# Optimization experiments

Hardware: AMD Instinct MI355X
Metric: run time of the kernel (lower is better)

Reference implementation:

```python
import jax, jax.numpy as jnp
import numpy as np
import math

B, S, E_PHI, E_F, H_F, N_HEADS = 2, 2048, 1024, 1024, 1024, 16


def setup_inputs() -> dict:
    key = jax.random.key(0)
    ks = jax.random.split(key, 7)
    return {
        "q": jax.random.normal(ks[0], (B, S, E_PHI), dtype=jnp.float32),
        "k": jax.random.normal(ks[1], (B, S, E_PHI), dtype=jnp.float32),
        "v": jax.random.normal(ks[2], (B, S, E_F), dtype=jnp.float32),
        # weights stored as [in, out]; applied as x @ W (same math as nn.Linear with W^T)
        "W_q": jax.random.normal(ks[3], (E_PHI, H_F), dtype=jnp.float32) * 0.02,
        "W_k": jax.random.normal(ks[4], (E_PHI, H_F), dtype=jnp.float32) * 0.02,
        "W_v": jax.random.normal(ks[5], (E_F, H_F), dtype=jnp.float32) * 0.02,
        "W_o": jax.random.normal(ks[6], (H_F, E_F), dtype=jnp.float32) * 0.02,
    }


def reference(q, k, v, W_q, W_k, W_v, W_o):
    Bq, Sq, _ = q.shape
    Dh = H_F // N_HEADS
    scale = 1.0 / math.sqrt(H_F)
    # projections -> [B, H, S, Dh]
    qh = (q @ W_q).reshape(Bq, Sq, N_HEADS, Dh).transpose(0, 2, 1, 3)
    kh = (k @ W_k).reshape(Bq, Sq, N_HEADS, Dh).transpose(0, 2, 1, 3)
    vh = (v @ W_v).reshape(Bq, Sq, N_HEADS, Dh).transpose(0, 2, 1, 3)
    # near-causal mask: mask out j >= i (triu incl. diagonal), EXCEPT position [0,0]
    mask = jnp.triu(jnp.ones((Sq, Sq), dtype=bool), 0).at[0, 0].set(False)
    scores = jnp.einsum('bhsd,bhtd->bhst', qh, kh) * scale  # [B,H,S,S]
    scores = jnp.where(mask, -jnp.inf, scores)
    probs = jax.nn.softmax(scores, axis=-1)  # dropout = identity (eval mode)
    out = jnp.einsum('bhst,bhtd->bhsd', probs, vh)  # [B,H,S,Dh]
    out = out.transpose(0, 2, 1, 3).reshape(Bq, Sq, H_F)
    return out @ W_o
```

## Files before the change

### kernel.cpp

```cpp
#include <hip/hip_runtime.h>
#include <type_traits>

#define S_LEN 2048
#define NHEAD 16
#define DHEAD 64
#define EMB   1024
#define NBATCH 2

typedef __bf16 bf16_t;
typedef bf16_t bf16x8 __attribute__((ext_vector_type(8)));
typedef float  f32x4  __attribute__((ext_vector_type(4)));
typedef unsigned short us_t;
typedef us_t   us8    __attribute__((ext_vector_type(8)));
typedef us_t   us4    __attribute__((ext_vector_type(4)));
typedef unsigned int u32x4 __attribute__((ext_vector_type(4)));
typedef unsigned int u32x2 __attribute__((ext_vector_type(2)));
typedef short  s16x4  __attribute__((ext_vector_type(4)));

static __device__ __forceinline__ bf16x8 ld_bf16x8(const us_t* p) {
  return __builtin_bit_cast(bf16x8, *reinterpret_cast<const us8*>(p));
}
static __device__ __forceinline__ us_t f2bf(float f) {
  bf16_t h = (bf16_t)f;
  return __builtin_bit_cast(us_t, h);
}
static __device__ __forceinline__ unsigned cvt_pk_bf16(float lo, float hi) {
  unsigned r;
  asm("v_cvt_pk_bf16_f32 %0, %1, %2" : "=v"(r) : "v"(lo), "v"(hi));
  return r;
}
#if __has_builtin(__builtin_amdgcn_exp2f)
#define EXP2(x) __builtin_amdgcn_exp2f(x)
#else
#define EXP2(x) exp2f(x)
#endif
static __device__ __forceinline__ void gload16(const void* g, void* lds) {
  __builtin_amdgcn_global_load_lds((const __attribute__((address_space(1))) void*)g,
                                   (__attribute__((address_space(3))) void*)lds,
                                   16, 0, 0);
}

__global__ __launch_bounds__(256) void prep(const float* __restrict__ W0,
                                            const float* __restrict__ W1,
                                            const float* __restrict__ W2,
                                            const float* __restrict__ W3,
                                            us_t* __restrict__ T0,
                                            us_t* __restrict__ T1,
                                            us_t* __restrict__ T2,
                                            us_t* __restrict__ T3) {
  __shared__ float tile[32][33];
  const int z = blockIdx.z;
  const float* W = (z == 0) ? W0 : (z == 1) ? W1 : (z == 2) ? W2 : W3;
  us_t* WT = (z == 0) ? T0 : (z == 1) ? T1 : (z == 2) ? T2 : T3;
  const int n0 = blockIdx.x * 32, k0 = blockIdx.y * 32;
  const int tx = threadIdx.x & 31, ty = threadIdx.x >> 5;
#pragma unroll
  for (int i = 0; i < 32; i += 8)
    tile[ty + i][tx] = W[(size_t)(k0 + ty + i) * EMB + n0 + tx];
  __syncthreads();
#pragma unroll
  for (int i = 0; i < 32; i += 8)
    WT[(size_t)(n0 + ty + i) * EMB + k0 + tx] = f2bf(tile[tx][ty + i]);
}

template<int MODE, bool AF32>
static __device__ __forceinline__ void gemm_core(const void* __restrict__ Ap,
                                                 const us_t* __restrict__ BT,
                                                 void* __restrict__ O,
                                                 int mt, int nt,
                                                 char (*As)[8192], char (*Bs)[8192]) {
  const int lane = threadIdx.x & 63;
  const int wave = threadIdx.x >> 6;
  const int wm = (wave >> 1) * 64;
  const int wn = (wave & 1) * 64;
  const int lr = lane & 15;
  const int lg = lane >> 4;

  f32x4 acc[4][4] = {};
  f32x4 ar[2][2];

  auto a_load = [&](int k0) {
#pragma unroll
    for (int i = 0; i < 2; ++i) {
      const int seg = wave * 2 + i;
      const int r = seg * 16 + (lane >> 2);
      const float* ap = (const float*)Ap + (size_t)(mt * 128 + r) * EMB + k0 + (lane & 3) * 8;
      ar[i][0] = *reinterpret_cast<const f32x4*>(ap);
      ar[i][1] = *reinterpret_cast<const f32x4*>(ap + 4);
    }
  };
  auto a_write = [&](int buf) {
#pragma unroll
    for (int i = 0; i < 2; ++i) {
      const int seg = wave * 2 + i;
      u32x4 w = { cvt_pk_bf16(ar[i][0][0], ar[i][0][1]), cvt_pk_bf16(ar[i][0][2], ar[i][0][3]),
                  cvt_pk_bf16(ar[i][1][0], ar[i][1][1]), cvt_pk_bf16(ar[i][1][2], ar[i][1][3]) };
      *reinterpret_cast<u32x4*>(&As[buf][seg * 1024 + lane * 16]) = w;
    }
  };
  auto stage = [&](int buf, int k0) {
#pragma unroll
    for (int i = 0; i < 2; ++i) {
      const int seg = wave * 2 + i;
      const int r = seg * 16 + (lane >> 2);
      if constexpr (!AF32)
        gload16((const char*)Ap + ((size_t)(mt * 128 + r) * EMB + k0) * 2 + (lane & 3) * 16,
                &As[buf][seg * 1024]);
      gload16((const char*)BT + ((size_t)(nt * 128 + r) * EMB + k0) * 2 + (lane & 3) * 16,
              &Bs[buf][seg * 1024]);
    }
  };

  if constexpr (AF32) { a_load(0); stage(0, 0); a_write(0); }
  else stage(0, 0);
  __syncthreads();

  for (int ks = 0; ks < EMB / 32; ++ks) {
    const int cur = ks & 1;
    const bool more = (ks + 1 < EMB / 32);
    if (more) {
      if constexpr (AF32) a_load((ks + 1) * 32);
      stage(cur ^ 1, (ks + 1) * 32);
    }
    bf16x8 af[4], bfr[4];
#pragma unroll
    for (int i = 0; i < 4; ++i)
      af[i] = ld_bf16x8((const us_t*)&As[cur][(wm + 16 * i + lr) * 64 + lg * 16]);
#pragma unroll
    for (int j = 0; j < 4; ++j)
      bfr[j] = ld_bf16x8((const us_t*)&Bs[cur][(wn + 16 * j + lr) * 64 + lg * 16]);
#pragma unroll
    for (int i = 0; i < 4; ++i)
#pragma unroll
      for (int j = 0; j < 4; ++j)
        acc[i][j] = __builtin_amdgcn_mfma_f32_16x16x32_bf16(af[i], bfr[j], acc[i][j], 0, 0, 0);
    if (more) {
      if constexpr (AF32) a_write(cur ^ 1);
    }
    __syncthreads();
  }

  const int crow = (lane >> 4) * 4;
#pragma unroll
  for (int i = 0; i < 4; ++i)
#pragma unroll
    for (int j = 0; j < 4; ++j)
#pragma unroll
      for (int r = 0; r < 4; ++r) {
        const int m = mt * 128 + wm + 16 * i + crow + r;
        const int n = nt * 128 + wn + 16 * j + lr;
        const float val = acc[i][j][r];
        if constexpr (MODE == 2) {
          ((float*)O)[(size_t)m * EMB + n] = val;
        } else {
          us_t* o = (us_t*)O;
          const int b = m >> 11, s = m & (S_LEN - 1);
          const int h = n >> 6, d = n & 63;
          if constexpr (MODE == 0)
            o[(((size_t)(b * NHEAD + h) * S_LEN + s) << 6) + d] = f2bf(val);
          else
            o[((size_t)(b * NHEAD + h) * DHEAD + d) * S_LEN + s] = f2bf(val);
        }
      }
}

__global__ __launch_bounds__(256) void proj3(const float* __restrict__ A0,
                                             const float* __restrict__ A1,
                                             const float* __restrict__ A2,
                                             const us_t* __restrict__ B0,
                                             const us_t* __restrict__ B1,
                                             const us_t* __restrict__ B2,
                                             us_t* __restrict__ O0,
                                             us_t* __restrict__ O1,
                                             us_t* __restrict__ O2) {
  __shared__ char As[2][8192];
  __shared__ char Bs[2][8192];
  const int f = blockIdx.x;
  const int w = (f & 7) * 96 + (f >> 3);
  const int z = w >> 8;
  const int rem = w & 255;
  const int mt = rem >> 3, nt = rem & 7;
  const float* A = (z == 0) ? A0 : (z == 1) ? A1 : A2;
  const us_t* BT = (z == 0) ? B0 : (z == 1) ? B1 : B2;
  us_t* O = (z == 0) ? O0 : (z == 1) ? O1 : O2;
  if (z < 2)
    gemm_core<0, true>(A, BT, O, mt, nt, As, Bs);
  else
    gemm_core<1, true>(A, BT, O, mt, nt, As, Bs);
}

__global__ __launch_bounds__(256) void gemmout(const us_t* __restrict__ A,
                                               const us_t* __restrict__ BT,
                                               float* __restrict__ O) {
  __shared__ char As[2][8192];
  __shared__ char Bs[2][8192];
  const int f = blockIdx.x;
  const int w = (f & 7) * 32 + (f >> 3);
  const int mt = w >> 3, nt = w & 7;
  gemm_core<2, false>(A, BT, O, mt, nt, As, Bs);
}

__global__ __launch_bounds__(256, 4) void attn64(const us_t* __restrict__ Qh,
                                                 const us_t* __restrict__ Kh,
                                                 const us_t* __restrict__ Vt,
                                                 us_t* __restrict__ AO) {
  __shared__ char Ks[2][8192];
  __shared__ char Vs[2][8192];
  const int flat = blockIdx.y * 32 + blockIdx.x;
  const int bh = (flat & 7) * 4 + ((flat >> 3) & 3);
  const int g = flat >> 5;
  const int Q = g >> 3, p = g & 7;
  const int qt = (Q == 0) ? 31 - p : (Q == 1) ? 16 + p : (Q == 2) ? 15 - p : p;
  const int lane = threadIdx.x & 63;
  const int wave = threadIdx.x >> 6;
  const int lr = lane & 15;
  const int lg = lane >> 4;
  const int q_glob = qt * 64 + wave * 16 + lr;

  const us_t* qbase = Qh + ((size_t)bh * S_LEN + q_glob) * DHEAD;
  bf16x8 qf[2] = { ld_bf16x8(qbase + lg * 8), ld_bf16x8(qbase + 32 + lg * 8) };

  const us_t* kbase0 = Kh + (size_t)bh * S_LEN * DHEAD;
  const us_t* vbase0 = Vt + (size_t)bh * DHEAD * S_LEN;

  int koff[8];
#pragma unroll
  for (int ks = 0; ks < 2; ++ks)
#pragma unroll
    for (int j = 0; j < 4; ++j)
      koff[ks * 4 + j] = (16 * j + lr) * 128 + ((ks * 64 + lg * 16) ^ ((lr & 7) << 4));
  int voff[16];
#pragma unroll
  for (int jk = 0; jk < 4; ++jk)
#pragma unroll
    for (int jd = 0; jd < 4; ++jd)
      voff[jk * 4 + jd] = (16 * jd + lr) * 128 + ((32 * jk + 8 * lg) ^ ((lr & 7) << 4));

  auto stage = [&](int buf, int t0) {
#pragma unroll
    for (int i = 0; i < 2; ++i) {
      const int seg = wave * 2 + i;
      const int r = seg * 8 + (lane >> 3);
      const int c16 = (lane & 7) ^ (lane >> 3);
      gload16(kbase0 + (size_t)(t0 + r) * DHEAD + c16 * 8, &Ks[buf][seg * 1024]);
      gload16(vbase0 + (size_t)r * S_LEN + t0 + c16 * 8, &Vs[buf][seg * 1024]);
    }
  };

  f32x4 oaccT[4] = {};
  float mrow = -1e9f;
  float lsum = 0.f;
  const float c = 0.045084220f;

  stage(0, 0);
  __syncthreads();

  for (int tt = 0; tt <= qt; ++tt) {
    const int cur = tt & 1;
    if (tt < qt) stage(cur ^ 1, (tt + 1) * 64);

    f32x4 sc[4] = {};
    __builtin_amdgcn_s_setprio(1);
#pragma unroll
    for (int ks = 0; ks < 2; ++ks)
#pragma unroll
      for (int j = 0; j < 4; ++j) {
        bf16x8 ak = ld_bf16x8((const us_t*)&Ks[cur][koff[ks * 4 + j]]);
        sc[j] = __builtin_amdgcn_mfma_f32_16x16x32_bf16(ak, qf[ks], sc[j], 0, 0, 0);
      }
    __builtin_amdgcn_s_setprio(0);

    if (tt == qt) {
#pragma unroll
      for (int j = 0; j < 4; ++j)
#pragma unroll
        for (int r = 0; r < 4; ++r) {
          const int t_g = tt * 64 + 16 * j + 4 * lg + r;
          if (!((t_g < q_glob) || (q_glob == 0 && t_g == 0))) sc[j][r] = -1e30f;
        }
    }

    float mx = sc[0][0];
#pragma unroll
    for (int j = 0; j < 4; ++j)
#pragma unroll
      for (int r = 0; r < 4; ++r) mx = fmaxf(mx, sc[j][r]);
    const float mxc = mx * c;
    if (__any(mxc > mrow + 8.f)) {
      float mc = mxc;
      mc = fmaxf(mc, __shfl_xor(mc, 16, 64));
      mc = fmaxf(mc, __shfl_xor(mc, 32, 64));
      const float m2 = fmaxf(mrow, mc);
      const float alpha = EXP2(mrow - m2);
      lsum *= alpha;
#pragma unroll
      for (int j = 0; j < 4; ++j)
#pragma unroll
        for (int r = 0; r < 4; ++r) oaccT[j][r] *= alpha;
      mrow = m2;
    }

    unsigned int pk[4][2];
    float ps = 0.f;
#pragma unroll
    for (int j = 0; j < 4; ++j) {
      float p0 = EXP2(__builtin_fmaf(sc[j][0], c, -mrow));
      float p1 = EXP2(__builtin_fmaf(sc[j][1], c, -mrow));
      float p2 = EXP2(__builtin_fmaf(sc[j][2], c, -mrow));
      float p3 = EXP2(__builtin_fmaf(sc[j][3], c, -mrow));
      ps += (p0 + p1) + (p2 + p3);
      pk[j][0] = cvt_pk_bf16(p0, p1);
      pk[j][1] = cvt_pk_bf16(p2, p3);
    }
    lsum += ps;

    __builtin_amdgcn_s_setprio(1);
#pragma unroll
    for (int jk = 0; jk < 4; ++jk) {
      s16x4 pf = __builtin_bit_cast(s16x4, (u32x2){pk[jk][0], pk[jk][1]});
#pragma unroll
      for (int jd = 0; jd < 4; ++jd) {
        s16x4 av = __builtin_bit_cast(s16x4,
            *reinterpret_cast<const us4*>(&Vs[cur][voff[jk * 4 + jd]]));
        oaccT[jd] = __builtin_amdgcn_mfma_f32_16x16x16bf16_1k(av, pf, oaccT[jd], 0, 0, 0);
      }
    }
    __builtin_amdgcn_s_setprio(0);
    __syncthreads();
  }

  lsum += __shfl_xor(lsum, 16, 64);
  lsum += __shfl_xor(lsum, 32, 64);
  const float inv = 1.0f / lsum;
  const int b = bh >> 4, h = bh & 15;
  us_t* aout = AO + (size_t)(b * S_LEN + q_glob) * EMB + h * DHEAD;
#pragma unroll
  for (int j = 0; j < 4; ++j) {
    us4 w;
#pragma unroll
    for (int r = 0; r < 4; ++r) w[r] = f2bf(oaccT[j][r] * inv);
    *reinterpret_cast<us4*>(aout + 16 * j + 4 * lg) = w;
  }
}

extern "C" void kernel_launch(void* const* d_in, const int* in_sizes, int n_in,
                              void* d_out, int out_size, void* d_ws, size_t ws_size,
                              hipStream_t stream) {
  const float* q  = (const float*)d_in[0];
  const float* k  = (const float*)d_in[1];
  const float* v  = (const float*)d_in[2];
  const float* Wq = (const float*)d_in[3];
  const float* Wk = (const float*)d_in[4];
  const float* Wv = (const float*)d_in[5];
  const float* Wo = (const float*)d_in[6];
  float* out = (float*)d_out;

  char* ws = (char*)d_ws;
  const size_t MB = 1024 * 1024;
  us_t* WqT = (us_t*)(ws + 0 * MB);
  us_t* WkT = (us_t*)(ws + 2 * MB);
  us_t* WvT = (us_t*)(ws + 4 * MB);
  us_t* WoT = (us_t*)(ws + 6 * MB);
  us_t* Qh  = (us_t*)(ws + 8 * MB);
  us_t* Kh  = (us_t*)(ws + 16 * MB);
  us_t* Vt  = (us_t*)(ws + 24 * MB);
  us_t* AO  = (us_t*)(ws + 32 * MB);

  prep<<<dim3(32, 32, 4), 256, 0, stream>>>(Wq, Wk, Wv, Wo, WqT, WkT, WvT, WoT);

  proj3<<<768, 256, 0, stream>>>(q, k, v, WqT, WkT, WvT, Qh, Kh, Vt);

  attn64<<<dim3(32, 32), 256, 0, stream>>>(Qh, Kh, Vt, AO);

  gemmout<<<256, 256, 0, stream>>>(AO, WoT, out);
}
```

Measured before the change: 123.9 us.

## Deepen fp32-A projection GEMM pipeline with explicit waitcnt and barriers

```diff
diff --git a/kernel.cpp b/kernel.cpp
--- a/kernel.cpp
+++ b/kernel.cpp
@@ -77,9 +77,26 @@
   const int lg = lane >> 4;
 
   f32x4 acc[4][4] = {};
-  f32x4 ar[2][2];
-
-  auto a_load = [&](int k0) {
+
+  auto stageB = [&](int buf, int k0) {
+#pragma unroll
+    for (int i = 0; i < 2; ++i) {
+      const int seg = wave * 2 + i;
+      const int r = seg * 16 + (lane >> 2);
+      gload16((const char*)BT + ((size_t)(nt * 128 + r) * EMB + k0) * 2 + (lane & 3) * 16,
+              &Bs[buf][seg * 1024]);
+    }
+  };
+  auto stageA = [&](int buf, int k0) {
+#pragma unroll
+    for (int i = 0; i < 2; ++i) {
+      const int seg = wave * 2 + i;
+      const int r = seg * 16 + (lane >> 2);
+      gload16((const char*)Ap + ((size_t)(mt * 128 + r) * EMB + k0) * 2 + (lane & 3) * 16,
+              &As[buf][seg * 1024]);
+    }
+  };
+  auto a_load = [&](f32x4 (&ar)[2][2], int k0) {
 #pragma unroll
     for (int i = 0; i < 2; ++i) {
       const int seg = wave * 2 + i;
@@ -89,7 +106,7 @@
       ar[i][1] = *reinterpret_cast<const f32x4*>(ap + 4);
     }
   };
-  auto a_write = [&](int buf) {
+  auto a_write = [&](f32x4 (&ar)[2][2], int buf) {
 #pragma unroll
     for (int i = 0; i < 2; ++i) {
       const int seg = wave * 2 + i;
@@ -98,46 +115,88 @@
       *reinterpret_cast<u32x4*>(&As[buf][seg * 1024 + lane * 16]) = w;
     }
   };
-  auto stage = [&](int buf, int k0) {
-#pragma unroll
-    for (int i = 0; i < 2; ++i) {
-      const int seg = wave * 2 + i;
-      const int r = seg * 16 + (lane >> 2);
-      if constexpr (!AF32)
-        gload16((const char*)Ap + ((size_t)(mt * 128 + r) * EMB + k0) * 2 + (lane & 3) * 16,
-                &As[buf][seg * 1024]);
-      gload16((const char*)BT + ((size_t)(nt * 128 + r) * EMB + k0) * 2 + (lane & 3) * 16,
-              &Bs[buf][seg * 1024]);
-    }
-  };
-
-  if constexpr (AF32) { a_load(0); stage(0, 0); a_write(0); }
-  else stage(0, 0);
-  __syncthreads();
-
-  for (int ks = 0; ks < EMB / 32; ++ks) {
-    const int cur = ks & 1;
-    const bool more = (ks + 1 < EMB / 32);
-    if (more) {
-      if constexpr (AF32) a_load((ks + 1) * 32);
-      stage(cur ^ 1, (ks + 1) * 32);
-    }
+  auto mfma_step = [&](int buf) {
     bf16x8 af[4], bfr[4];
 #pragma unroll
     for (int i = 0; i < 4; ++i)
-      af[i] = ld_bf16x8((const us_t*)&As[cur][(wm + 16 * i + lr) * 64 + lg * 16]);
+      af[i] = ld_bf16x8((const us_t*)&As[buf][(wm + 16 * i + lr) * 64 + lg * 16]);
 #pragma unroll
     for (int j = 0; j < 4; ++j)
-      bfr[j] = ld_bf16x8((const us_t*)&Bs[cur][(wn + 16 * j + lr) * 64 + lg * 16]);
+      bfr[j] = ld_bf16x8((const us_t*)&Bs[buf][(wn + 16 * j + lr) * 64 + lg * 16]);
 #pragma unroll
     for (int i = 0; i < 4; ++i)
 #pragma unroll
       for (int j = 0; j < 4; ++j)
         acc[i][j] = __builtin_amdgcn_mfma_f32_16x16x32_bf16(af[i], bfr[j], acc[i][j], 0, 0, 0);
-    if (more) {
-      if constexpr (AF32) a_write(cur ^ 1);
-    }
+  };
+
+  if constexpr (AF32) {
+    f32x4 arE[2][2], arO[2][2];
+    a_load(arE, 0);
+    stageB(0, 0);
+    a_write(arE, 0);
+    a_load(arO, 32);
+    asm volatile("s_waitcnt vmcnt(4)" ::: "memory");
+    asm volatile("s_waitcnt lgkmcnt(0)" ::: "memory");
+    __builtin_amdgcn_s_barrier();
+    __builtin_amdgcn_sched_barrier(0);
+
+#pragma unroll 1
+    for (int ks = 0; ks < EMB / 32 - 4; ks += 2) {
+      stageB(1, (ks + 1) * 32);
+      mfma_step(0);
+      a_write(arO, 1);
+      a_load(arE, (ks + 2) * 32);
+      asm volatile("s_waitcnt vmcnt(4)" ::: "memory");
+      asm volatile("s_waitcnt lgkmcnt(0)" ::: "memory");
+      __builtin_amdgcn_s_barrier();
+      __builtin_amdgcn_sched_barrier(0);
+      stageB(0, (ks + 2) * 32);
+      mfma_step(1);
+      a_write(arE, 0);
+      a_load(arO, (ks + 3) * 32);
+      asm volatile("s_waitcnt vmcnt(4)" ::: "memory");
+      asm volatile("s_waitcnt lgkmcnt(0)" ::: "memory");
+      __builtin_amdgcn_s_barrier();
+      __builtin_amdgcn_sched_barrier(0);
+    }
+    stageB(1, 29 * 32);
+    mfma_step(0);
+    a_write(arO, 1);
+    a_load(arE, 30 * 32);
+    asm volatile("s_waitcnt vmcnt(4)" ::: "memory");
+    asm volatile("s_waitcnt lgkmcnt(0)" ::: "memory");
+    __builtin_amdgcn_s_barrier();
+    __builtin_amdgcn_sched_barrier(0);
+
+    stageB(0, 30 * 32);
+    mfma_step(1);
+    a_write(arE, 0);
+    a_load(arO, 31 * 32);
+    asm volatile("s_waitcnt vmcnt(4)" ::: "memory");
+    asm volatile("s_waitcnt lgkmcnt(0)" ::: "memory");
+    __builtin_amdgcn_s_barrier();
+    __builtin_amdgcn_sched_barrier(0);
+
+    stageB(1, 31 * 32);
+    mfma_step(0);
+    a_write(arO, 1);
+    asm volatile("s_waitcnt vmcnt(0)" ::: "memory");
+    asm volatile("s_waitcnt lgkmcnt(0)" ::: "memory");
+    __builtin_amdgcn_s_barrier();
+    __builtin_amdgcn_sched_barrier(0);
+
+    mfma_step(1);
+  } else {
+    stageA(0, 0);
+    stageB(0, 0);
     __syncthreads();
+    for (int ks = 0; ks < EMB / 32; ++ks) {
+      const int cur = ks & 1;
+      if (ks + 1 < EMB / 32) { stageA(cur ^ 1, (ks + 1) * 32); stageB(cur ^ 1, (ks + 1) * 32); }
+      mfma_step(cur);
+      __syncthreads();
+    }
   }
 
   const int crow = (lane >> 4) * 4;
@@ -164,15 +223,15 @@
       }
 }
 
-__global__ __launch_bounds__(256) void proj3(const float* __restrict__ A0,
-                                             const float* __restrict__ A1,
-                                             const float* __restrict__ A2,
-                                             const us_t* __restrict__ B0,
-                                             const us_t* __restrict__ B1,
-                                             const us_t* __restrict__ B2,
-                                             us_t* __restrict__ O0,
-                                             us_t* __restrict__ O1,
-                                             us_t* __restrict__ O2) {
+__global__ __launch_bounds__(256, 3) void proj3(const float* __restrict__ A0,
+                                                const float* __restrict__ A1,
+                                                const float* __restrict__ A2,
+                                                const us_t* __restrict__ B0,
+                                                const us_t* __restrict__ B1,
+                                                const us_t* __restrict__ B2,
+                                                us_t* __restrict__ O0,
+                                                us_t* __restrict__ O1,
+                                                us_t* __restrict__ O2) {
   __shared__ char As[2][8192];
   __shared__ char Bs[2][8192];
   const int f = blockIdx.x;
```

New measurement: 122.0 us. About the same (-1.5%).
